# Kernel tuning notes

Measured on AMD Instinct MI355X. Metric: run time of the kernel, lower is better.

The kernel has to match this reference:

```python
import jax, jax.numpy as jnp
import numpy as np

T, B, D_MODEL, H, FFN = 2048, 2, 128, 8, 1024
EPS = 1e-5
NEG = -1e9


def setup_inputs() -> dict:
    key = jax.random.key(0)
    ks = jax.random.split(key, 20)
    d = D_MODEL
    w = lambda k, sh: (jax.random.normal(k, sh, jnp.float32) * 0.02)
    z = lambda n: jnp.zeros((n,), jnp.float32)
    o = lambda n: jnp.ones((n,), jnp.float32)
    return {
        "x": jax.random.normal(ks[0], (T, B, d), jnp.float32),
        "enc": jax.random.normal(ks[1], (T, B, d), jnp.float32),
        "sa_wq": w(ks[2], (d, d)), "sa_bq": z(d),
        "sa_wk": w(ks[3], (d, d)), "sa_bk": z(d),
        "sa_wv": w(ks[4], (d, d)), "sa_bv": z(d),
        "sa_wo": w(ks[5], (d, d)), "sa_bo": z(d),
        "ln1_g": o(d), "ln1_b": z(d),
        "ca_wq": w(ks[6], (d, d)), "ca_bq": z(d),
        "ca_wk": w(ks[7], (d, d)), "ca_bk": z(d),
        "ca_wv": w(ks[8], (d, d)), "ca_bv": z(d),
        "ca_wo": w(ks[9], (d, d)), "ca_bo": z(d),
        "ln2_g": o(d), "ln2_b": z(d),
        "fc1_w": w(ks[10], (d, FFN)), "fc1_b": z(FFN),
        "fc2_w": w(ks[11], (FFN, d)), "fc2_b": z(d),
        "ln3_g": o(d), "ln3_b": z(d),
    }


def _ln(x, g, b):
    m = jnp.mean(x, -1, keepdims=True)
    v = jnp.mean(jnp.square(x - m), -1, keepdims=True)
    return (x - m) * jax.lax.rsqrt(v + EPS) * g + b


def _mha(q_in, kv_in, wq, bq, wk, bk, wv, bv, wo, bo, mask):
    # q_in: [T, B, C]; kv_in: [S, B, C]  (Time x Batch x Channel, as in torch src)
    Tq, Bz, C = q_in.shape
    S = kv_in.shape[0]
    Dh = C // H
    q = (q_in @ wq + bq) * (Dh ** -0.5)
    k = kv_in @ wk + bk
    v = kv_in @ wv + bv
    q = q.reshape(Tq, Bz, H, Dh)
    k = k.reshape(S, Bz, H, Dh)
    v = v.reshape(S, Bz, H, Dh)
    scores = jnp.einsum('tbhd,sbhd->bhts', q, k)  # materialized [B,H,T,S]
    if mask is not None:
        scores = scores + mask  # additive causal mask, broadcast over b,h
    probs = jax.nn.softmax(scores, axis=-1)
    out = jnp.einsum('bhts,sbhd->tbhd', probs, v).reshape(Tq, Bz, C)
    return out @ wo + bo


def reference(x, enc,
              sa_wq, sa_bq, sa_wk, sa_bk, sa_wv, sa_bv, sa_wo, sa_bo,
              ln1_g, ln1_b,
              ca_wq, ca_bq, ca_wk, ca_bk, ca_wv, ca_bv, ca_wo, ca_bo,
              ln2_g, ln2_b,
              fc1_w, fc1_b, fc2_w, fc2_b,
              ln3_g, ln3_b):
    Tq = x.shape[0]
    causal = jnp.where(jnp.tril(jnp.ones((Tq, Tq), bool)), 0.0, NEG).astype(x.dtype)
    # self-attention block (post-norm, dropout=0 in eval)
    res = x
    x = res + _mha(x, x, sa_wq, sa_bq, sa_wk, sa_bk, sa_wv, sa_bv, sa_wo, sa_bo, causal)
    x = _ln(x, ln1_g, ln1_b)
    # cross-attention block
    res = x
    x = res + _mha(x, enc, ca_wq, ca_bq, ca_wk, ca_bk, ca_wv, ca_bv, ca_wo, ca_bo, None)
    x = _ln(x, ln2_g, ln2_b)
    # FFN block (exact erf gelu, matching torch F.gelu default)
    res = x
    h = jax.nn.gelu(x @ fc1_w + fc1_b, approximate=False)
    x = res + (h @ fc2_w + fc2_b)
    x = _ln(x, ln3_g, ln3_b)
    return x
```

## Files before the change

kernel.cpp:

```cpp
#include <hip/hip_runtime.h>
#include <hip/hip_bf16.h>

#define TT 2048
#define BB 2
#define DM 128
#define HH 8
#define DH 16
#define FFN_N 1024
#define ROWS (TT * BB)
#define EPS_LN 1e-5f
#define NC 8
#define SC (TT / NC)
#define NQ32 (TT / 32)
#define NQP (TT / 64)
#define NBH (BB * HH)

typedef __attribute__((ext_vector_type(8))) short bf16x8;
typedef __attribute__((ext_vector_type(4))) short bf16x4v;
typedef __attribute__((ext_vector_type(4))) float f32x4;
typedef __attribute__((ext_vector_type(16))) float f32x16;

__device__ __forceinline__ short f2bf(float x) {
    __hip_bfloat16 h = __float2bfloat16(x);
    union { __hip_bfloat16 hh; short s; } u; u.hh = h; return u.s;
}

__global__ __launch_bounds__(256) void cvt_w_all(
    const float* w0, const float* w1, const float* w2, const float* w3,
    const float* w4, const float* w5, const float* w6, const float* w7,
    const float* w8, const float* w9,
    short* o0, short* o1, short* o2, short* o3,
    short* o4, short* o5, short* o6, short* o7,
    short* o8, short* o9)
{
    const float* srcs[10] = {w0, w1, w2, w3, w4, w5, w6, w7, w8, w9};
    short* dsts[10] = {o0, o1, o2, o3, o4, o5, o6, o7, o8, o9};
    const int bx = blockIdx.x;
    int wi, tile, K, N;
    if (bx < 128)      { wi = bx >> 4; tile = bx & 15;  K = 128;  N = 128;  }
    else if (bx < 256) { wi = 8;       tile = bx - 128; K = 128;  N = 1024; }
    else               { wi = 9;       tile = bx - 256; K = 1024; N = 128;  }
    const float* src = srcs[wi];
    short* dst = dsts[wi];
    const int ntx = N >> 5;
    const int k0 = (tile / ntx) << 5;
    const int n0 = (tile % ntx) << 5;

    __shared__ float sm[32][33];
    const int j = threadIdx.x & 31;
    const int i0 = threadIdx.x >> 5;
    #pragma unroll
    for (int p = 0; p < 4; ++p) {
        const int ii = i0 + p * 8;
        sm[ii][j] = src[(size_t)(k0 + ii) * N + n0 + j];
    }
    __syncthreads();
    #pragma unroll
    for (int p = 0; p < 4; ++p) {
        const int ii = i0 + p * 8;
        dst[(size_t)(n0 + ii) * K + k0 + j] = f2bf(sm[j][ii]);
    }
}

template<int MODE, int GELU>
__global__ __launch_bounds__(256) void gemm_mfma(
    const short* __restrict__ A, const short* __restrict__ Wt,
    const float* __restrict__ bias, void* __restrict__ outp,
    int M, int N, int K, float scale)
{
    const int tid = threadIdx.x;
    const int w = tid >> 6, lane = tid & 63;
    const int wm = w >> 1, wn = w & 1;
    const int g = lane >> 4, qi = lane & 15;
    const int bm = blockIdx.y * 64 + wm * 32;
    const int bn = blockIdx.x * 64 + wn * 32;

    f32x4 acc[2][2];
    #pragma unroll
    for (int a = 0; a < 2; ++a)
        #pragma unroll
        for (int b = 0; b < 2; ++b) acc[a][b] = (f32x4){0.f, 0.f, 0.f, 0.f};

    for (int k0 = 0; k0 < K; k0 += 32) {
        bf16x8 af[2], bf[2];
        #pragma unroll
        for (int fm = 0; fm < 2; ++fm) {
            const short* p = A + (size_t)(bm + fm * 16 + qi) * K + k0 + g * 4;
            bf16x4v lo = *(const bf16x4v*)p;
            bf16x4v hi = *(const bf16x4v*)(p + 16);
            af[fm][0] = lo[0]; af[fm][1] = lo[1]; af[fm][2] = lo[2]; af[fm][3] = lo[3];
            af[fm][4] = hi[0]; af[fm][5] = hi[1]; af[fm][6] = hi[2]; af[fm][7] = hi[3];
        }
        #pragma unroll
        for (int fn = 0; fn < 2; ++fn) {
            const short* p = Wt + (size_t)(bn + fn * 16 + qi) * K + k0 + g * 4;
            bf16x4v lo = *(const bf16x4v*)p;
            bf16x4v hi = *(const bf16x4v*)(p + 16);
            bf[fn][0] = lo[0]; bf[fn][1] = lo[1]; bf[fn][2] = lo[2]; bf[fn][3] = lo[3];
            bf[fn][4] = hi[0]; bf[fn][5] = hi[1]; bf[fn][6] = hi[2]; bf[fn][7] = hi[3];
        }
        #pragma unroll
        for (int fm = 0; fm < 2; ++fm)
            #pragma unroll
            for (int fn = 0; fn < 2; ++fn)
                acc[fm][fn] = __builtin_amdgcn_mfma_f32_16x16x32_bf16(
                    af[fm], bf[fn], acc[fm][fn], 0, 0, 0);
    }

    #pragma unroll
    for (int fm = 0; fm < 2; ++fm)
        #pragma unroll
        for (int fn = 0; fn < 2; ++fn)
            #pragma unroll
            for (int r = 0; r < 4; ++r) {
                const int m = bm + fm * 16 + g * 4 + r;
                const int n = bn + fn * 16 + qi;
                float v = (acc[fm][fn][r] + bias[n]) * scale;
                if (GELU) v = 0.5f * v * (1.f + erff(v * 0.70710678118654752f));
                ((short*)outp)[(size_t)m * N + n] = f2bf(v);
            }
}

__global__ __launch_bounds__(256) void qkv5(
    const float* __restrict__ x, const float* __restrict__ enc,
    const short* __restrict__ W0, const short* __restrict__ W1, const short* __restrict__ W2,
    const short* __restrict__ W3, const short* __restrict__ W4,
    const float* __restrict__ B0, const float* __restrict__ B1, const float* __restrict__ B2,
    const float* __restrict__ B3, const float* __restrict__ B4,
    short* __restrict__ O0, short* __restrict__ O1, short* __restrict__ O2,
    short* __restrict__ O3, short* __restrict__ O4, float s0)
{
    const int z = blockIdx.z;
    const float* A = (z < 3) ? x : enc;
    const short* Wt = (z == 0) ? W0 : (z == 1) ? W1 : (z == 2) ? W2 : (z == 3) ? W3 : W4;
    const float* bias = (z == 0) ? B0 : (z == 1) ? B1 : (z == 2) ? B2 : (z == 3) ? B3 : B4;
    short* out = (z == 0) ? O0 : (z == 1) ? O1 : (z == 2) ? O2 : (z == 3) ? O3 : O4;
    const float scale = (z == 0) ? s0 : 1.f;
    const int vmode = (z == 2 || z == 4);
    const int K = DM, N = DM;

    const int tid = threadIdx.x;
    const int w = tid >> 6, lane = tid & 63;
    const int wm = w >> 1, wn = w & 1;
    const int g = lane >> 4, qi = lane & 15;
    const int bm = blockIdx.y * 64 + wm * 32;
    const int bn = blockIdx.x * 64 + wn * 32;

    f32x4 acc[2][2];
    #pragma unroll
    for (int a = 0; a < 2; ++a)
        #pragma unroll
        for (int b = 0; b < 2; ++b) acc[a][b] = (f32x4){0.f, 0.f, 0.f, 0.f};

    for (int k0 = 0; k0 < K; k0 += 32) {
        bf16x8 af[2], bf[2];
        #pragma unroll
        for (int fm = 0; fm < 2; ++fm) {
            const float* p = A + (size_t)(bm + fm * 16 + qi) * K + k0 + g * 4;
            float4 lo = *(const float4*)p;
            float4 hi = *(const float4*)(p + 16);
            af[fm][0] = f2bf(lo.x); af[fm][1] = f2bf(lo.y); af[fm][2] = f2bf(lo.z); af[fm][3] = f2bf(lo.w);
            af[fm][4] = f2bf(hi.x); af[fm][5] = f2bf(hi.y); af[fm][6] = f2bf(hi.z); af[fm][7] = f2bf(hi.w);
        }
        #pragma unroll
        for (int fn = 0; fn < 2; ++fn) {
            const short* p = Wt + (size_t)(bn + fn * 16 + qi) * K + k0 + g * 4;
            bf16x4v lo = *(const bf16x4v*)p;
            bf16x4v hi = *(const bf16x4v*)(p + 16);
            bf[fn][0] = lo[0]; bf[fn][1] = lo[1]; bf[fn][2] = lo[2]; bf[fn][3] = lo[3];
            bf[fn][4] = hi[0]; bf[fn][5] = hi[1]; bf[fn][6] = hi[2]; bf[fn][7] = hi[3];
        }
        #pragma unroll
        for (int fm = 0; fm < 2; ++fm)
            #pragma unroll
            for (int fn = 0; fn < 2; ++fn)
                acc[fm][fn] = __builtin_amdgcn_mfma_f32_16x16x32_bf16(
                    af[fm], bf[fn], acc[fm][fn], 0, 0, 0);
    }

    #pragma unroll
    for (int fm = 0; fm < 2; ++fm)
        #pragma unroll
        for (int fn = 0; fn < 2; ++fn)
            #pragma unroll
            for (int r = 0; r < 4; ++r) {
                const int m = bm + fm * 16 + g * 4 + r;
                const int n = bn + fn * 16 + qi;
                const float v = (acc[fm][fn][r] + bias[n]) * scale;
                const int t = m >> 1, bz = m & 1, hH = n >> 4, d = n & 15;
                size_t idx;
                if (!vmode) {
                    const int dp = ((d >> 2) & 1) * 8 + (d & 3) + ((d >> 3) & 1) * 4;
                    idx = ((size_t)(bz * HH + hH) * TT + t) * DH + dp;
                } else {
                    const int u = t & 15;
                    const int tp = (t & ~15) | (((u >> 2) & 1) * 8 + (u & 3) + ((u >> 3) & 1) * 4);
                    idx = ((size_t)(bz * HH + hH) * DH + d) * TT + tp;
                }
                out[idx] = f2bf(v);
            }
}

template<int CAUSAL>
__global__ __launch_bounds__(256, 4) void attn_part(
    const short* __restrict__ Qh, const short* __restrict__ Kh,
    const short* __restrict__ Vt, float* __restrict__ pacc,
    float* __restrict__ pml)
{
    const int wv = threadIdx.x >> 6;
    const int lane = threadIdx.x & 63;
    const int tsk = blockIdx.x * 4 + wv;
    const int bh = tsk >> 8;
    const int rr = tsk & 255;
    const int c = rr & (NC - 1);
    const int qp0 = rr >> 3;
    const int qp = (qp0 * 13 + c * 5) & (NQP - 1);
    const int qtA = qp * 64;
    const int qtB = qtA + 32;
    const int start = c * SC;
    const int send = CAUSAL ? min(start + SC, qtB + 32) : (start + SC);
    if (CAUSAL && start >= send) return;

    const int q = lane & 31;
    const int h = lane >> 5;

    const bf16x8 qf1 = *(const bf16x8*)(Qh + ((size_t)bh * TT + qtA + q) * DH + h * 8);
    const bf16x8 qf2 = *(const bf16x8*)(Qh + ((size_t)bh * TT + qtB + q) * DH + h * 8);

    f32x16 acc1, acc2;
    #pragma unroll
    for (int i = 0; i < 16; ++i) { acc1[i] = 0.f; acc2[i] = 0.f; }
    float l1 = 0.f, l2 = 0.f;

    for (int sb = start; sb < send; sb += 32) {
        const bf16x8 kf = *(const bf16x8*)(Kh + ((size_t)bh * TT + sb + q) * DH + h * 8);
        f32x16 z;
        #pragma unroll
        for (int i = 0; i < 16; ++i) z[i] = 0.f;
        f32x16 s1 = __builtin_amdgcn_mfma_f32_32x32x16_bf16(kf, qf1, z, 0, 0, 0);
        f32x16 s2 = __builtin_amdgcn_mfma_f32_32x32x16_bf16(kf, qf2, z, 0, 0, 0);

        if (CAUSAL && (sb + 31 > qtA)) {
            #pragma unroll
            for (int r = 0; r < 16; ++r) {
                const int s_glob = sb + (r & 3) + 8 * (r >> 2) + 4 * h;
                if (s_glob > qtA + q) s1[r] = -1.0e30f;
                if (s_glob > qtB + q) s2[r] = -1.0e30f;
            }
        }

        float c1 = 0.f, c2 = 0.f;
        #pragma unroll
        for (int i = 0; i < 16; ++i) {
            const float p1 = exp2f(s1[i]);
            const float p2 = exp2f(s2[i]);
            s1[i] = p1; s2[i] = p2;
            c1 += p1; c2 += p2;
        }
        l1 += c1; l2 += c2;

        #pragma unroll
        for (int j = 0; j < 2; ++j) {
            bf16x8 pf1, pf2;
            #pragma unroll
            for (int e = 0; e < 8; ++e) { pf1[e] = f2bf(s1[8 * j + e]); pf2[e] = f2bf(s2[8 * j + e]); }
            const bf16x8 vf = *(const bf16x8*)(Vt + ((size_t)bh * DH + q) * TT + sb + 16 * j + h * 8);
            acc1 = __builtin_amdgcn_mfma_f32_32x32x16_bf16(pf1, vf, acc1, 0, 0, 0);
            acc2 = __builtin_amdgcn_mfma_f32_32x32x16_bf16(pf2, vf, acc2, 0, 0, 0);
        }
    }

    l1 += __shfl_xor(l1, 32);
    l2 += __shfl_xor(l2, 32);

    const size_t tA = ((size_t)bh * NQ32 + qp * 2) * NC + c;
    const size_t tB = ((size_t)bh * NQ32 + qp * 2 + 1) * NC + c;
    const int d = q;
    if (d < 16) {
        float* pb1 = pacc + tA * 512 + (size_t)d * 32;
        float* pb2 = pacc + tB * 512 + (size_t)d * 32;
        *(f32x4*)(pb1 + 4 * h)      = (f32x4){acc1[0],  acc1[1],  acc1[2],  acc1[3]};
        *(f32x4*)(pb1 + 8 + 4 * h)  = (f32x4){acc1[4],  acc1[5],  acc1[6],  acc1[7]};
        *(f32x4*)(pb1 + 16 + 4 * h) = (f32x4){acc1[8],  acc1[9],  acc1[10], acc1[11]};
        *(f32x4*)(pb1 + 24 + 4 * h) = (f32x4){acc1[12], acc1[13], acc1[14], acc1[15]};
        *(f32x4*)(pb2 + 4 * h)      = (f32x4){acc2[0],  acc2[1],  acc2[2],  acc2[3]};
        *(f32x4*)(pb2 + 8 + 4 * h)  = (f32x4){acc2[4],  acc2[5],  acc2[6],  acc2[7]};
        *(f32x4*)(pb2 + 16 + 4 * h) = (f32x4){acc2[8],  acc2[9],  acc2[10], acc2[11]};
        *(f32x4*)(pb2 + 24 + 4 * h) = (f32x4){acc2[12], acc2[13], acc2[14], acc2[15]};
    }
    if (h == 0) {
        pml[tA * 32 + q] = l1;
        pml[tB * 32 + q] = l2;
    }
}

__global__ __launch_bounds__(256) void attn_merge(
    const float* __restrict__ pacc, const float* __restrict__ pml,
    short* __restrict__ outb, int causal)
{
    const int wv = threadIdx.x >> 6;
    const int lane = threadIdx.x & 63;
    const int task2 = blockIdx.x * 4 + wv;
    const int qt32 = task2 & (NQ32 - 1);
    const int bh = task2 >> 6;
    const int bz = bh / HH, head = bh % HH;
    const int qt = qt32 * 32;
    const int q = lane & 31, h = lane >> 5;
    const int qp = qt32 >> 1;
    const int nc = causal ? min(NC, (qp * 64 + 64 + SC - 1) / SC) : NC;
    const size_t base = (size_t)task2 * NC;

    float L = 0.f;
    float o[8] = {0.f, 0.f, 0.f, 0.f, 0.f, 0.f, 0.f, 0.f};
    for (int c = 0; c < nc; ++c) {
        L += pml[(base + c) * 32 + q];
        const float* pb = pacc + (base + c) * 512 + (size_t)h * 8 * 32 + q;
        #pragma unroll
        for (int dd = 0; dd < 8; ++dd) o[dd] += pb[dd * 32];
    }

    const float inv = 1.f / L;
    short* op = outb + ((size_t)(qt + q) * BB + bz) * DM + head * DH + h * 8;
    bf16x8 ov;
    #pragma unroll
    for (int dd = 0; dd < 8; ++dd) ov[dd] = f2bf(o[dd] * inv);
    *(bf16x8*)op = ov;
}

template<int KSTEPS, int QPROJ>
__global__ __launch_bounds__(256) void lngemm(
    const short* __restrict__ A, const short* __restrict__ Wt,
    const float* __restrict__ bias, const float* __restrict__ resid,
    const float* __restrict__ lg, const float* __restrict__ lb,
    float* __restrict__ outF, short* __restrict__ outB,
    const short* __restrict__ Wq, const float* __restrict__ bq,
    short* __restrict__ Oq, float qs)
{
    const int tid = threadIdx.x;
    const int w = tid >> 6;
    const int lane = tid & 63;
    const int ch = w & 1, kh = w >> 1;
    const int gq = lane >> 4, qi = lane & 15;
    const int m0 = blockIdx.x * 16;
    const int K = KSTEPS * 32;
    const int KH = KSTEPS / 2;

    __shared__ float part[16][130];
    __shared__ float smean[2][16], ssq[2][16];
    __shared__ short Alds[16][136];

    f32x4 acc[4];
    #pragma unroll
    for (int fn = 0; fn < 4; ++fn) acc[fn] = (f32x4){0.f, 0.f, 0.f, 0.f};

    for (int ks = kh * KH; ks < kh * KH + KH; ++ks) {
        const int k0 = ks * 32;
        bf16x8 af;
        {
            const short* p = A + (size_t)(m0 + qi) * K + k0 + gq * 4;
            bf16x4v lo = *(const bf16x4v*)p;
            bf16x4v hi = *(const bf16x4v*)(p + 16);
            af[0] = lo[0]; af[1] = lo[1]; af[2] = lo[2]; af[3] = lo[3];
            af[4] = hi[0]; af[5] = hi[1]; af[6] = hi[2]; af[7] = hi[3];
        }
        #pragma unroll
        for (int fn = 0; fn < 4; ++fn) {
            const short* p = Wt + (size_t)(ch * 64 + fn * 16 + qi) * K + k0 + gq * 4;
            bf16x4v lo = *(const bf16x4v*)p;
            bf16x4v hi = *(const bf16x4v*)(p + 16);
            bf16x8 bf;
            bf[0] = lo[0]; bf[1] = lo[1]; bf[2] = lo[2]; bf[3] = lo[3];
            bf[4] = hi[0]; bf[5] = hi[1]; bf[6] = hi[2]; bf[7] = hi[3];
            acc[fn] = __builtin_amdgcn_mfma_f32_16x16x32_bf16(af, bf, acc[fn], 0, 0, 0);
        }
    }

    if (kh == 1) {
        #pragma unroll
        for (int fn = 0; fn < 4; ++fn)
            #pragma unroll
            for (int r = 0; r < 4; ++r)
                part[gq * 4 + r][ch * 64 + fn * 16 + qi] = acc[fn][r];
    }
    __syncthreads();

    float vv[4][4];
    if (kh == 0) {
        #pragma unroll
        for (int fn = 0; fn < 4; ++fn) {
            const int n = ch * 64 + fn * 16 + qi;
            const float bn = bias[n];
            #pragma unroll
            for (int r = 0; r < 4; ++r) {
                const int m = m0 + gq * 4 + r;
                vv[fn][r] = acc[fn][r] + part[gq * 4 + r][n] + bn
                          + resid[(size_t)m * DM + n];
            }
        }
        float ps[4], pq[4];
        #pragma unroll
        for (int r = 0; r < 4; ++r) {
            float s = 0.f, q2 = 0.f;
            #pragma unroll
            for (int fn = 0; fn < 4; ++fn) { s += vv[fn][r]; q2 += vv[fn][r] * vv[fn][r]; }
            #pragma unroll
            for (int off = 1; off < 16; off <<= 1) {
                s += __shfl_xor(s, off);
                q2 += __shfl_xor(q2, off);
            }
            ps[r] = s; pq[r] = q2;
        }
        if (qi == 0) {
            #pragma unroll
            for (int r = 0; r < 4; ++r) {
                smean[ch][gq * 4 + r] = ps[r];
                ssq[ch][gq * 4 + r] = pq[r];
            }
        }
    }
    __syncthreads();

    if (kh == 0) {
        #pragma unroll
        for (int r = 0; r < 4; ++r) {
            const int row = gq * 4 + r;
            const int m = m0 + row;
            const float mean = (smean[0][row] + smean[1][row]) * (1.f / DM);
            const float var = (ssq[0][row] + ssq[1][row]) * (1.f / DM) - mean * mean;
            const float rstd = rsqrtf(var + EPS_LN);
            #pragma unroll
            for (int fn = 0; fn < 4; ++fn) {
                const int n = ch * 64 + fn * 16 + qi;
                const float val = (vv[fn][r] - mean) * rstd * lg[n] + lb[n];
                outF[(size_t)m * DM + n] = val;
                const short vb = f2bf(val);
                if (outB) outB[(size_t)m * DM + n] = vb;
                if (QPROJ) Alds[row][n] = vb;
            }
        }
    }

    if (QPROJ) {
        __syncthreads();
        f32x4 qacc[2];
        qacc[0] = (f32x4){0.f, 0.f, 0.f, 0.f};
        qacc[1] = (f32x4){0.f, 0.f, 0.f, 0.f};
        for (int ks = 0; ks < 4; ++ks) {
            const int k0 = ks * 32;
            bf16x8 af;
            {
                const short* p = &Alds[qi][k0 + gq * 4];
                af[0] = p[0]; af[1] = p[1]; af[2] = p[2]; af[3] = p[3];
                af[4] = p[16]; af[5] = p[17]; af[6] = p[18]; af[7] = p[19];
            }
            #pragma unroll
            for (int fn = 0; fn < 2; ++fn) {
                const short* p = Wq + (size_t)(w * 32 + fn * 16 + qi) * DM + k0 + gq * 4;
                bf16x4v lo = *(const bf16x4v*)p;
                bf16x4v hi = *(const bf16x4v*)(p + 16);
                bf16x8 bf;
                bf[0] = lo[0]; bf[1] = lo[1]; bf[2] = lo[2]; bf[3] = lo[3];
                bf[4] = hi[0]; bf[5] = hi[1]; bf[6] = hi[2]; bf[7] = hi[3];
                qacc[fn] = __builtin_amdgcn_mfma_f32_16x16x32_bf16(af, bf, qacc[fn], 0, 0, 0);
            }
        }
        #pragma unroll
        for (int fn = 0; fn < 2; ++fn)
            #pragma unroll
            for (int r = 0; r < 4; ++r) {
                const int m = m0 + gq * 4 + r;
                const int n = w * 32 + fn * 16 + qi;
                const float v = (qacc[fn][r] + bq[n]) * qs;
                const int t = m >> 1, bz = m & 1, hH = n >> 4, d = n & 15;
                const int dp = ((d >> 2) & 1) * 8 + (d & 3) + ((d >> 3) & 1) * 4;
                Oq[((size_t)(bz * HH + hH) * TT + t) * DH + dp] = f2bf(v);
            }
    }
}

extern "C" void kernel_launch(void* const* d_in, const int* in_sizes, int n_in,
                              void* d_out, int out_size, void* d_ws, size_t ws_size,
                              hipStream_t stream)
{
    const float* x     = (const float*)d_in[0];
    const float* enc   = (const float*)d_in[1];
    const float* sa_wq = (const float*)d_in[2];
    const float* sa_bq = (const float*)d_in[3];
    const float* sa_wk = (const float*)d_in[4];
    const float* sa_bk = (const float*)d_in[5];
    const float* sa_wv = (const float*)d_in[6];
    const float* sa_bv = (const float*)d_in[7];
    const float* sa_wo = (const float*)d_in[8];
    const float* sa_bo = (const float*)d_in[9];
    const float* ln1_g = (const float*)d_in[10];
    const float* ln1_b = (const float*)d_in[11];
    const float* ca_wq = (const float*)d_in[12];
    const float* ca_bq = (const float*)d_in[13];
    const float* ca_wk = (const float*)d_in[14];
    const float* ca_bk = (const float*)d_in[15];
    const float* ca_wv = (const float*)d_in[16];
    const float* ca_bv = (const float*)d_in[17];
    const float* ca_wo = (const float*)d_in[18];
    const float* ca_bo = (const float*)d_in[19];
    const float* ln2_g = (const float*)d_in[20];
    const float* ln2_b = (const float*)d_in[21];
    const float* fc1_w = (const float*)d_in[22];
    const float* fc1_b = (const float*)d_in[23];
    const float* fc2_w = (const float*)d_in[24];
    const float* fc2_b = (const float*)d_in[25];
    const float* ln3_g = (const float*)d_in[26];
    const float* ln3_b = (const float*)d_in[27];

    float* out = (float*)d_out;
    char* ws = (char*)d_ws;

    const size_t NE = (size_t)ROWS * DM;
    float* b5   = (float*)ws;    ws += NE * 4;
    float* b6   = (float*)ws;    ws += NE * 4;
    float* pacc = (float*)ws;    ws += (size_t)NBH * NQ32 * NC * 512 * 4;
    float* pml  = (float*)ws;    ws += (size_t)NBH * NQ32 * NC * 64 * 4;
    short* b6b  = (short*)ws;    ws += NE * 2;
    short* b3b  = (short*)ws;    ws += NE * 2;
    short* qh   = (short*)ws;    ws += NE * 2;
    short* kh   = (short*)ws;    ws += NE * 2 + 4096;
    short* vt   = (short*)ws;    ws += NE * 2 + 132 * 1024;
    short* kh2  = (short*)ws;    ws += NE * 2 + 4096;
    short* vt2  = (short*)ws;    ws += NE * 2 + 132 * 1024;
    short* hb   = (short*)ws;    ws += (size_t)ROWS * FFN_N * 2;
    short* wt_saq = (short*)ws;  ws += DM * DM * 2;
    short* wt_sak = (short*)ws;  ws += DM * DM * 2;
    short* wt_sav = (short*)ws;  ws += DM * DM * 2;
    short* wt_sao = (short*)ws;  ws += DM * DM * 2;
    short* wt_caq = (short*)ws;  ws += DM * DM * 2;
    short* wt_cak = (short*)ws;  ws += DM * DM * 2;
    short* wt_cav = (short*)ws;  ws += DM * DM * 2;
    short* wt_cao = (short*)ws;  ws += DM * DM * 2;
    short* wt_fc1 = (short*)ws;  ws += DM * FFN_N * 2;
    short* wt_fc2 = (short*)ws;  ws += FFN_N * DM * 2;

    const float qscale = 0.25f * 1.4426950408889634f;
    const dim3 qkvgrid(DM / 64, ROWS / 64, 5);
    const dim3 partgrid(NBH * NQP * NC / 4);
    const dim3 mergegrid(NBH * NQ32 / 4);
    const dim3 lngrid(ROWS / 16);
    const dim3 fc1grid(FFN_N / 64, ROWS / 64);

    hipLaunchKernelGGL(cvt_w_all, dim3(384), dim3(256), 0, stream,
                       sa_wq, sa_wk, sa_wv, sa_wo, ca_wq, ca_wk, ca_wv, ca_wo, fc1_w, fc2_w,
                       wt_saq, wt_sak, wt_sav, wt_sao, wt_caq, wt_cak, wt_cav, wt_cao, wt_fc1, wt_fc2);
    hipLaunchKernelGGL(qkv5, qkvgrid, dim3(256), 0, stream,
                       x, enc, wt_saq, wt_sak, wt_sav, wt_cak, wt_cav,
                       sa_bq, sa_bk, sa_bv, ca_bk, ca_bv,
                       qh, kh, vt, kh2, vt2, qscale);
    hipLaunchKernelGGL((attn_part<1>), partgrid, dim3(256), 0, stream,
                       qh, kh, vt, pacc, pml);
    hipLaunchKernelGGL(attn_merge, mergegrid, dim3(256), 0, stream, pacc, pml, b3b, 1);
    hipLaunchKernelGGL((lngemm<4, 1>), lngrid, dim3(256), 0, stream,
                       b3b, wt_sao, sa_bo, x, ln1_g, ln1_b, b5, (short*)nullptr,
                       wt_caq, ca_bq, qh, qscale);
    hipLaunchKernelGGL((attn_part<0>), partgrid, dim3(256), 0, stream,
                       qh, kh2, vt2, pacc, pml);
    hipLaunchKernelGGL(attn_merge, mergegrid, dim3(256), 0, stream, pacc, pml, b3b, 0);
    hipLaunchKernelGGL((lngemm<4, 0>), lngrid, dim3(256), 0, stream,
                       b3b, wt_cao, ca_bo, b5, ln2_g, ln2_b, b6, b6b,
                       (const short*)nullptr, (const float*)nullptr, (short*)nullptr, 1.f);
    hipLaunchKernelGGL((gemm_mfma<1, 1>), fc1grid, dim3(256), 0, stream,
                       b6b, wt_fc1, fc1_b, hb, ROWS, FFN_N, DM, 1.f);
    hipLaunchKernelGGL((lngemm<32, 0>), lngrid, dim3(256), 0, stream,
                       hb, wt_fc2, fc2_b, b6, ln3_g, ln3_b, out, (short*)nullptr,
                       (const short*)nullptr, (const float*)nullptr, (short*)nullptr, 1.f);
}
```

Baseline: 138.5 us.

## Fuse attention merge into LN-GEMM and fuse FFN fc1/fc2 into one kernel

Folds the attention partial-merge into the output-projection + layernorm kernel, so the merged attention rows are built in LDS instead of written to a bf16 buffer and read back. Replaces the separate fc1 GEMM and the fc2+LN kernel with one 512-thread kernel. Each block computes a 16x1024 GELU hidden tile in LDS and feeds it straight into fc2, a split-K reduction and layernorm. This removes two launches and the 8 MB hidden round-trip through global memory. In exchange, each block re-reads the full fc1/fc2 weights, and the large LDS footprint with small 16-row tiles may limit occupancy.

```diff
diff --git a/kernel.cpp b/kernel.cpp
--- a/kernel.cpp
+++ b/kernel.cpp
@@ -62,65 +62,6 @@
     }
 }
 
-template<int MODE, int GELU>
-__global__ __launch_bounds__(256) void gemm_mfma(
-    const short* __restrict__ A, const short* __restrict__ Wt,
-    const float* __restrict__ bias, void* __restrict__ outp,
-    int M, int N, int K, float scale)
-{
-    const int tid = threadIdx.x;
-    const int w = tid >> 6, lane = tid & 63;
-    const int wm = w >> 1, wn = w & 1;
-    const int g = lane >> 4, qi = lane & 15;
-    const int bm = blockIdx.y * 64 + wm * 32;
-    const int bn = blockIdx.x * 64 + wn * 32;
-
-    f32x4 acc[2][2];
-    #pragma unroll
-    for (int a = 0; a < 2; ++a)
-        #pragma unroll
-        for (int b = 0; b < 2; ++b) acc[a][b] = (f32x4){0.f, 0.f, 0.f, 0.f};
-
-    for (int k0 = 0; k0 < K; k0 += 32) {
-        bf16x8 af[2], bf[2];
-        #pragma unroll
-        for (int fm = 0; fm < 2; ++fm) {
-            const short* p = A + (size_t)(bm + fm * 16 + qi) * K + k0 + g * 4;
-            bf16x4v lo = *(const bf16x4v*)p;
-            bf16x4v hi = *(const bf16x4v*)(p + 16);
-            af[fm][0] = lo[0]; af[fm][1] = lo[1]; af[fm][2] = lo[2]; af[fm][3] = lo[3];
-            af[fm][4] = hi[0]; af[fm][5] = hi[1]; af[fm][6] = hi[2]; af[fm][7] = hi[3];
-        }
-        #pragma unroll
-        for (int fn = 0; fn < 2; ++fn) {
-            const short* p = Wt + (size_t)(bn + fn * 16 + qi) * K + k0 + g * 4;
-            bf16x4v lo = *(const bf16x4v*)p;
-            bf16x4v hi = *(const bf16x4v*)(p + 16);
-            bf[fn][0] = lo[0]; bf[fn][1] = lo[1]; bf[fn][2] = lo[2]; bf[fn][3] = lo[3];
-            bf[fn][4] = hi[0]; bf[fn][5] = hi[1]; bf[fn][6] = hi[2]; bf[fn][7] = hi[3];
-        }
-        #pragma unroll
-        for (int fm = 0; fm < 2; ++fm)
-            #pragma unroll
-            for (int fn = 0; fn < 2; ++fn)
-                acc[fm][fn] = __builtin_amdgcn_mfma_f32_16x16x32_bf16(
-                    af[fm], bf[fn], acc[fm][fn], 0, 0, 0);
-    }
-
-    #pragma unroll
-    for (int fm = 0; fm < 2; ++fm)
-        #pragma unroll
-        for (int fn = 0; fn < 2; ++fn)
-            #pragma unroll
-            for (int r = 0; r < 4; ++r) {
-                const int m = bm + fm * 16 + g * 4 + r;
-                const int n = bn + fn * 16 + qi;
-                float v = (acc[fm][fn][r] + bias[n]) * scale;
-                if (GELU) v = 0.5f * v * (1.f + erff(v * 0.70710678118654752f));
-                ((short*)outp)[(size_t)m * N + n] = f2bf(v);
-            }
-}
-
 __global__ __launch_bounds__(256) void qkv5(
     const float* __restrict__ x, const float* __restrict__ enc,
     const short* __restrict__ W0, const short* __restrict__ W1, const short* __restrict__ W2,
@@ -294,78 +235,72 @@
     }
 }
 
-__global__ __launch_bounds__(256) void attn_merge(
-    const float* __restrict__ pacc, const float* __restrict__ pml,
-    short* __restrict__ outb, int causal)
-{
-    const int wv = threadIdx.x >> 6;
-    const int lane = threadIdx.x & 63;
-    const int task2 = blockIdx.x * 4 + wv;
-    const int qt32 = task2 & (NQ32 - 1);
-    const int bh = task2 >> 6;
-    const int bz = bh / HH, head = bh % HH;
-    const int qt = qt32 * 32;
-    const int q = lane & 31, h = lane >> 5;
-    const int qp = qt32 >> 1;
-    const int nc = causal ? min(NC, (qp * 64 + 64 + SC - 1) / SC) : NC;
-    const size_t base = (size_t)task2 * NC;
-
-    float L = 0.f;
-    float o[8] = {0.f, 0.f, 0.f, 0.f, 0.f, 0.f, 0.f, 0.f};
-    for (int c = 0; c < nc; ++c) {
-        L += pml[(base + c) * 32 + q];
-        const float* pb = pacc + (base + c) * 512 + (size_t)h * 8 * 32 + q;
-        #pragma unroll
-        for (int dd = 0; dd < 8; ++dd) o[dd] += pb[dd * 32];
-    }
-
-    const float inv = 1.f / L;
-    short* op = outb + ((size_t)(qt + q) * BB + bz) * DM + head * DH + h * 8;
-    bf16x8 ov;
-    #pragma unroll
-    for (int dd = 0; dd < 8; ++dd) ov[dd] = f2bf(o[dd] * inv);
-    *(bf16x8*)op = ov;
-}
-
-template<int KSTEPS, int QPROJ>
-__global__ __launch_bounds__(256) void lngemm(
-    const short* __restrict__ A, const short* __restrict__ Wt,
-    const float* __restrict__ bias, const float* __restrict__ resid,
+template<int QPROJ>
+__global__ __launch_bounds__(256) void lnmerge(
+    const float* __restrict__ pacc, const float* __restrict__ pml, int causal,
+    const short* __restrict__ Wt, const float* __restrict__ bias,
+    const float* __restrict__ resid,
     const float* __restrict__ lg, const float* __restrict__ lb,
     float* __restrict__ outF, short* __restrict__ outB,
     const short* __restrict__ Wq, const float* __restrict__ bq,
     short* __restrict__ Oq, float qs)
 {
     const int tid = threadIdx.x;
+    const int m0 = blockIdx.x * 16;
+    const int t0 = m0 >> 1;
+    const int qt32 = t0 >> 5;
+    const int qp = qt32 >> 1;
+    const int nc = causal ? min(NC, (qp * 64 + 64 + SC - 1) / SC) : NC;
+
+    __shared__ short Alds[16][136];
+    __shared__ short Qlds[16][136];
+    __shared__ float part[16][130];
+    __shared__ float smean[2][16], ssq[2][16];
+
+    {
+        const int row = tid >> 4;
+        const int u = tid & 15;
+        const int m = m0 + row;
+        const int t = m >> 1, bz = m & 1;
+        const int q = t & 31;
+        const int h = u >> 1;
+        const int d0 = (u & 1) * 8;
+        const size_t base = ((size_t)(bz * HH + h) * NQ32 + qt32) * NC;
+        float L = 0.f;
+        float o[8] = {0.f, 0.f, 0.f, 0.f, 0.f, 0.f, 0.f, 0.f};
+        for (int c = 0; c < nc; ++c) {
+            L += pml[(base + c) * 32 + q];
+            const float* pb = pacc + (base + c) * 512 + (size_t)d0 * 32 + q;
+            #pragma unroll
+            for (int dd = 0; dd < 8; ++dd) o[dd] += pb[dd * 32];
+        }
+        const float inv = 1.f / L;
+        #pragma unroll
+        for (int dd = 0; dd < 8; ++dd)
+            Alds[row][h * DH + d0 + dd] = f2bf(o[dd] * inv);
+    }
+    __syncthreads();
+
     const int w = tid >> 6;
     const int lane = tid & 63;
     const int ch = w & 1, kh = w >> 1;
     const int gq = lane >> 4, qi = lane & 15;
-    const int m0 = blockIdx.x * 16;
-    const int K = KSTEPS * 32;
-    const int KH = KSTEPS / 2;
-
-    __shared__ float part[16][130];
-    __shared__ float smean[2][16], ssq[2][16];
-    __shared__ short Alds[16][136];
 
     f32x4 acc[4];
     #pragma unroll
     for (int fn = 0; fn < 4; ++fn) acc[fn] = (f32x4){0.f, 0.f, 0.f, 0.f};
 
-    for (int ks = kh * KH; ks < kh * KH + KH; ++ks) {
+    for (int ks = kh * 2; ks < kh * 2 + 2; ++ks) {
         const int k0 = ks * 32;
         bf16x8 af;
         {
-            const short* p = A + (size_t)(m0 + qi) * K + k0 + gq * 4;
-            bf16x4v lo = *(const bf16x4v*)p;
-            bf16x4v hi = *(const bf16x4v*)(p + 16);
-            af[0] = lo[0]; af[1] = lo[1]; af[2] = lo[2]; af[3] = lo[3];
-            af[4] = hi[0]; af[5] = hi[1]; af[6] = hi[2]; af[7] = hi[3];
+            const short* p = &Alds[qi][k0 + gq * 4];
+            af[0] = p[0]; af[1] = p[1]; af[2] = p[2]; af[3] = p[3];
+            af[4] = p[16]; af[5] = p[17]; af[6] = p[18]; af[7] = p[19];
         }
         #pragma unroll
         for (int fn = 0; fn < 4; ++fn) {
-            const short* p = Wt + (size_t)(ch * 64 + fn * 16 + qi) * K + k0 + gq * 4;
+            const short* p = Wt + (size_t)(ch * 64 + fn * 16 + qi) * DM + k0 + gq * 4;
             bf16x4v lo = *(const bf16x4v*)p;
             bf16x4v hi = *(const bf16x4v*)(p + 16);
             bf16x8 bf;
@@ -435,7 +370,7 @@
                 outF[(size_t)m * DM + n] = val;
                 const short vb = f2bf(val);
                 if (outB) outB[(size_t)m * DM + n] = vb;
-                if (QPROJ) Alds[row][n] = vb;
+                if (QPROJ) Qlds[row][n] = vb;
             }
         }
     }
@@ -449,7 +384,7 @@
             const int k0 = ks * 32;
             bf16x8 af;
             {
-                const short* p = &Alds[qi][k0 + gq * 4];
+                const short* p = &Qlds[qi][k0 + gq * 4];
                 af[0] = p[0]; af[1] = p[1]; af[2] = p[2]; af[3] = p[3];
                 af[4] = p[16]; af[5] = p[17]; af[6] = p[18]; af[7] = p[19];
             }
@@ -475,6 +410,151 @@
                 const int dp = ((d >> 2) & 1) * 8 + (d & 3) + ((d >> 3) & 1) * 4;
                 Oq[((size_t)(bz * HH + hH) * TT + t) * DH + dp] = f2bf(v);
             }
+    }
+}
+
+__global__ __launch_bounds__(512) void ffn_fused(
+    const short* __restrict__ A,
+    const short* __restrict__ W1t, const float* __restrict__ b1,
+    const short* __restrict__ W2t, const float* __restrict__ b2,
+    const float* __restrict__ resid,
+    const float* __restrict__ lg, const float* __restrict__ lb,
+    float* __restrict__ outF)
+{
+    const int tid = threadIdx.x;
+    const int w = tid >> 6, lane = tid & 63;
+    const int gq = lane >> 4, qi = lane & 15;
+    const int m0 = blockIdx.x * 16;
+
+    __shared__ short hlds[16][1032];
+    __shared__ float part[3][16][130];
+    __shared__ float smean[2][16], ssq[2][16];
+
+    {
+        f32x4 acc[8];
+        #pragma unroll
+        for (int fn = 0; fn < 8; ++fn) acc[fn] = (f32x4){0.f, 0.f, 0.f, 0.f};
+        for (int ks = 0; ks < 4; ++ks) {
+            const int k0 = ks * 32;
+            bf16x8 af;
+            {
+                const short* p = A + (size_t)(m0 + qi) * DM + k0 + gq * 4;
+                bf16x4v lo = *(const bf16x4v*)p;
+                bf16x4v hi = *(const bf16x4v*)(p + 16);
+                af[0] = lo[0]; af[1] = lo[1]; af[2] = lo[2]; af[3] = lo[3];
+                af[4] = hi[0]; af[5] = hi[1]; af[6] = hi[2]; af[7] = hi[3];
+            }
+            #pragma unroll
+            for (int fn = 0; fn < 8; ++fn) {
+                const short* p = W1t + (size_t)(w * 128 + fn * 16 + qi) * DM + k0 + gq * 4;
+                bf16x4v lo = *(const bf16x4v*)p;
+                bf16x4v hi = *(const bf16x4v*)(p + 16);
+                bf16x8 bf;
+                bf[0] = lo[0]; bf[1] = lo[1]; bf[2] = lo[2]; bf[3] = lo[3];
+                bf[4] = hi[0]; bf[5] = hi[1]; bf[6] = hi[2]; bf[7] = hi[3];
+                acc[fn] = __builtin_amdgcn_mfma_f32_16x16x32_bf16(af, bf, acc[fn], 0, 0, 0);
+            }
+        }
+        #pragma unroll
+        for (int fn = 0; fn < 8; ++fn) {
+            const int n = w * 128 + fn * 16 + qi;
+            const float bn = b1[n];
+            #pragma unroll
+            for (int r = 0; r < 4; ++r) {
+                float v = acc[fn][r] + bn;
+                v = 0.5f * v * (1.f + erff(v * 0.70710678118654752f));
+                hlds[gq * 4 + r][n] = f2bf(v);
+            }
+        }
+    }
+    __syncthreads();
+
+    const int ch = w & 1, kh = w >> 1;
+
+    f32x4 acc2[4];
+    #pragma unroll
+    for (int fn = 0; fn < 4; ++fn) acc2[fn] = (f32x4){0.f, 0.f, 0.f, 0.f};
+
+    for (int ks = kh * 8; ks < kh * 8 + 8; ++ks) {
+        const int k0 = ks * 32;
+        bf16x8 af;
+        {
+            const short* p = &hlds[qi][k0 + gq * 4];
+            af[0] = p[0]; af[1] = p[1]; af[2] = p[2]; af[3] = p[3];
+            af[4] = p[16]; af[5] = p[17]; af[6] = p[18]; af[7] = p[19];
+        }
+        #pragma unroll
+        for (int fn = 0; fn < 4; ++fn) {
+            const short* p = W2t + (size_t)(ch * 64 + fn * 16 + qi) * FFN_N + k0 + gq * 4;
+            bf16x4v lo = *(const bf16x4v*)p;
+            bf16x4v hi = *(const bf16x4v*)(p + 16);
+            bf16x8 bf;
+            bf[0] = lo[0]; bf[1] = lo[1]; bf[2] = lo[2]; bf[3] = lo[3];
+            bf[4] = hi[0]; bf[5] = hi[1]; bf[6] = hi[2]; bf[7] = hi[3];
+            acc2[fn] = __builtin_amdgcn_mfma_f32_16x16x32_bf16(af, bf, acc2[fn], 0, 0, 0);
+        }
+    }
+
+    if (kh >= 1) {
+        #pragma unroll
+        for (int fn = 0; fn < 4; ++fn)
+            #pragma unroll
+            for (int r = 0; r < 4; ++r)
+                part[kh - 1][gq * 4 + r][ch * 64 + fn * 16 + qi] = acc2[fn][r];
+    }
+    __syncthreads();
+
+    float vv[4][4];
+    if (kh == 0) {
+        #pragma unroll
+        for (int fn = 0; fn < 4; ++fn) {
+            const int n = ch * 64 + fn * 16 + qi;
+            const float bn = b2[n];
+            #pragma unroll
+            for (int r = 0; r < 4; ++r) {
+                const int row = gq * 4 + r;
+                const int m = m0 + row;
+                vv[fn][r] = acc2[fn][r] + part[0][row][n] + part[1][row][n]
+                          + part[2][row][n] + bn + resid[(size_t)m * DM + n];
+            }
+        }
+        float ps[4], pq[4];
+        #pragma unroll
+        for (int r = 0; r < 4; ++r) {
+            float s = 0.f, q2 = 0.f;
+            #pragma unroll
+            for (int fn = 0; fn < 4; ++fn) { s += vv[fn][r]; q2 += vv[fn][r] * vv[fn][r]; }
+            #pragma unroll
+            for (int off = 1; off < 16; off <<= 1) {
+                s += __shfl_xor(s, off);
+                q2 += __shfl_xor(q2, off);
+            }
+            ps[r] = s; pq[r] = q2;
+        }
+        if (qi == 0) {
+            #pragma unroll
+            for (int r = 0; r < 4; ++r) {
+                smean[ch][gq * 4 + r] = ps[r];
+                ssq[ch][gq * 4 + r] = pq[r];
+            }
+        }
+    }
+    __syncthreads();
+
+    if (kh == 0) {
+        #pragma unroll
+        for (int r = 0; r < 4; ++r) {
+            const int row = gq * 4 + r;
+            const int m = m0 + row;
+            const float mean = (smean[0][row] + smean[1][row]) * (1.f / DM);
+            const float var = (ssq[0][row] + ssq[1][row]) * (1.f / DM) - mean * mean;
+            const float rstd = rsqrtf(var + EPS_LN);
+            #pragma unroll
+            for (int fn = 0; fn < 4; ++fn) {
+                const int n = ch * 64 + fn * 16 + qi;
+                outF[(size_t)m * DM + n] = (vv[fn][r] - mean) * rstd * lg[n] + lb[n];
+            }
+        }
     }
 }
 
@@ -520,13 +600,11 @@
     float* pacc = (float*)ws;    ws += (size_t)NBH * NQ32 * NC * 512 * 4;
     float* pml  = (float*)ws;    ws += (size_t)NBH * NQ32 * NC * 64 * 4;
     short* b6b  = (short*)ws;    ws += NE * 2;
-    short* b3b  = (short*)ws;    ws += NE * 2;
     short* qh   = (short*)ws;    ws += NE * 2;
     short* kh   = (short*)ws;    ws += NE * 2 + 4096;
     short* vt   = (short*)ws;    ws += NE * 2 + 132 * 1024;
     short* kh2  = (short*)ws;    ws += NE * 2 + 4096;
     short* vt2  = (short*)ws;    ws += NE * 2 + 132 * 1024;
-    short* hb   = (short*)ws;    ws += (size_t)ROWS * FFN_N * 2;
     short* wt_saq = (short*)ws;  ws += DM * DM * 2;
     short* wt_sak = (short*)ws;  ws += DM * DM * 2;
     short* wt_sav = (short*)ws;  ws += DM * DM * 2;
@@ -541,9 +619,7 @@
     const float qscale = 0.25f * 1.4426950408889634f;
     const dim3 qkvgrid(DM / 64, ROWS / 64, 5);
     const dim3 partgrid(NBH * NQP * NC / 4);
-    const dim3 mergegrid(NBH * NQ32 / 4);
     const dim3 lngrid(ROWS / 16);
-    const dim3 fc1grid(FFN_N / 64, ROWS / 64);
 
     hipLaunchKernelGGL(cvt_w_all, dim3(384), dim3(256), 0, stream,
                        sa_wq, sa_wk, sa_wv, sa_wo, ca_wq, ca_wk, ca_wv, ca_wo, fc1_w, fc2_w,
@@ -554,19 +630,14 @@
                        qh, kh, vt, kh2, vt2, qscale);
     hipLaunchKernelGGL((attn_part<1>), partgrid, dim3(256), 0, stream,
                        qh, kh, vt, pacc, pml);
-    hipLaunchKernelGGL(attn_merge, mergegrid, dim3(256), 0, stream, pacc, pml, b3b, 1);
-    hipLaunchKernelGGL((lngemm<4, 1>), lngrid, dim3(256), 0, stream,
-                       b3b, wt_sao, sa_bo, x, ln1_g, ln1_b, b5, (short*)nullptr,
+    hipLaunchKernelGGL((lnmerge<1>), lngrid, dim3(256), 0, stream,
+                       pacc, pml, 1, wt_sao, sa_bo, x, ln1_g, ln1_b, b5, (short*)nullptr,
                        wt_caq, ca_bq, qh, qscale);
     hipLaunchKernelGGL((attn_part<0>), partgrid, dim3(256), 0, stream,
                        qh, kh2, vt2, pacc, pml);
-    hipLaunchKernelGGL(attn_merge, mergegrid, dim3(256), 0, stream, pacc, pml, b3b, 0);
-    hipLaunchKernelGGL((lngemm<4, 0>), lngrid, dim3(256), 0, stream,
-                       b3b, wt_cao, ca_bo, b5, ln2_g, ln2_b, b6, b6b,
+    hipLaunchKernelGGL((lnmerge<0>), lngrid, dim3(256), 0, stream,
+                       pacc, pml, 0, wt_cao, ca_bo, b5, ln2_g, ln2_b, b6, b6b,
                        (const short*)nullptr, (const float*)nullptr, (short*)nullptr, 1.f);
-    hipLaunchKernelGGL((gemm_mfma<1, 1>), fc1grid, dim3(256), 0, stream,
-                       b6b, wt_fc1, fc1_b, hb, ROWS, FFN_N, DM, 1.f);
-    hipLaunchKernelGGL((lngemm<32, 0>), lngrid, dim3(256), 0, stream,
-                       hb, wt_fc2, fc2_b, b6, ln3_g, ln3_b, out, (short*)nullptr,
-                       (const short*)nullptr, (const float*)nullptr, (short*)nullptr, 1.f);
+    hipLaunchKernelGGL(ffn_fused, lngrid, dim3(512), 0, stream,
+                       b6b, wt_fc1, fc1_b, wt_fc2, fc2_b, b6, ln3_g, ln3_b, out);
 }
```

After: 145.2 us. 1.05x slower.
